# Kernel tuning notes

Measured on AMD Instinct MI355X. Metric: run time of the kernel, lower is better.

## Reference

```python
import jax, jax.numpy as jnp
import numpy as np

E = 1024      # embedding_size
H = 16        # num_head
DQ = DK = DV = 64  # per-head q/k/v size


def setup_inputs() -> dict:
    key = jax.random.key(0)
    ks = jax.random.split(key, 9)
    B, S = 2, 2048
    s = 1.0 / np.sqrt(E)
    return {
        "q": jax.random.normal(ks[0], (B, S, E), jnp.float32),
        "k": jax.random.normal(ks[1], (B, S, E), jnp.float32),
        "v": jax.random.normal(ks[2], (B, S, E), jnp.float32),
        "w_q": jax.random.normal(ks[3], (E, H * DQ), jnp.float32) * s,
        "b_q": jax.random.normal(ks[4], (H * DQ,), jnp.float32) * s,
        "w_k": jax.random.normal(ks[5], (E, H * DK), jnp.float32) * s,
        "b_k": jax.random.normal(ks[6], (H * DK,), jnp.float32) * s,
        "w_v": jax.random.normal(ks[7], (E, H * DV), jnp.float32) * s,
        "b_v": jax.random.normal(ks[8], (H * DV,), jnp.float32) * s,
    }


def reference(q, k, v, w_q, b_q, w_k, b_k, w_v, b_v):
    B, Sq, _ = q.shape
    Sk = k.shape[1]
    # projections -> [B, S, H, d] -> [B, H, S, d]
    qh = (q @ w_q + b_q).reshape(B, Sq, H, DQ).transpose(0, 2, 1, 3)
    kh = (k @ w_k + b_k).reshape(B, Sk, H, DK).transpose(0, 2, 1, 3)
    vh = (v @ w_v + b_v).reshape(B, Sk, H, DV).transpose(0, 2, 1, 3)
    # scaled dot-product attention; scores [B, H, Sq, Sk]
    scores = jnp.einsum("bhqd,bhkd->bhqk", qh, kh) / jnp.sqrt(jnp.float32(DQ))
    weights = jax.nn.softmax(scores, axis=-1)
    out = jnp.einsum("bhqk,bhkd->bhqd", weights, vh)  # [B, H, Sq, DV]
    return out.transpose(0, 2, 1, 3).reshape(B, Sq, H * DV)
```

## Files before the change

### kernel.cpp

```cpp
#include <hip/hip_runtime.h>
#include <hip/hip_bf16.h>

typedef __bf16 bf16_t;
typedef bf16_t bf16x8 __attribute__((ext_vector_type(8)));
typedef bf16_t bf16x4 __attribute__((ext_vector_type(4)));
typedef short  short4v __attribute__((ext_vector_type(4)));
typedef float  f32x4  __attribute__((ext_vector_type(4)));

#define MFMA16(a,b,c) __builtin_amdgcn_mfma_f32_16x16x32_bf16(a, b, c, 0, 0, 0)

static __device__ inline f32x4 mfma_k16(bf16x4 a, bf16x4 b, f32x4 c) {
#if __has_builtin(__builtin_amdgcn_mfma_f32_16x16x16_bf16)
  return __builtin_amdgcn_mfma_f32_16x16x16_bf16(a, b, c, 0, 0, 0);
#else
  return __builtin_amdgcn_mfma_f32_16x16x16bf16_1k(
      __builtin_bit_cast(short4v, a), __builtin_bit_cast(short4v, b), c, 0, 0, 0);
#endif
}

constexpr int S = 2048, H = 16, Dh = 64;
constexpr int N = H * Dh;
constexpr int K = 1024;
constexpr float QSCALE = 0.125f * 1.4426950408889634f;

static __device__ inline void load_lds16(const bf16_t* g, bf16_t* l) {
  __builtin_amdgcn_global_load_lds(
      (const __attribute__((address_space(1))) void*)g,
      (__attribute__((address_space(3))) void*)l, 16, 0, 0);
}

static __device__ inline ushort f2bb(float x) {
  bf16_t h = (bf16_t)x;
  return __builtin_bit_cast(ushort, h);
}

__global__ __launch_bounds__(256) void prep(
    const float* __restrict__ q, const float* __restrict__ k,
    const float* __restrict__ v,
    const float* __restrict__ wq, const float* __restrict__ wk,
    const float* __restrict__ wv,
    bf16_t* __restrict__ xq, bf16_t* __restrict__ xk, bf16_t* __restrict__ xv,
    bf16_t* __restrict__ wtq, bf16_t* __restrict__ wtk, bf16_t* __restrict__ wtv) {
  __shared__ ushort tile[64][68];
  int bx = blockIdx.x, t = threadIdx.x;
  if (bx < 6144) {
    int z = bx >> 11, bb = bx & 2047;
    const float* xi = z == 0 ? q : z == 1 ? k : v;
    bf16_t*      xo = z == 0 ? xq : z == 1 ? xk : xv;
    size_t idx = ((size_t)bb * 256 + t) * 8;
    float4 a = *(const float4*)&xi[idx];
    float4 b = *(const float4*)&xi[idx + 4];
    bf16x8 w;
    w[0] = (bf16_t)a.x; w[1] = (bf16_t)a.y; w[2] = (bf16_t)a.z; w[3] = (bf16_t)a.w;
    w[4] = (bf16_t)b.x; w[5] = (bf16_t)b.y; w[6] = (bf16_t)b.z; w[7] = (bf16_t)b.w;
    *(bf16x8*)&xo[idx] = w;
  } else {
    int zz = bx - 6144;
    int z = zz >> 8, bb = zz & 255;
    const float* wi = z == 0 ? wq : z == 1 ? wk : wv;
    ushort*      wo = (ushort*)(z == 0 ? wtq : z == 1 ? wtk : wtv);
    int k0 = (bb >> 4) * 64, n0 = (bb & 15) * 64;
    for (int i = 0; i < 4; ++i) {
      int idx4 = (i * 256 + t) * 4;
      int r = idx4 >> 6, c = idx4 & 63;
      float4 vv = *(const float4*)&wi[(size_t)(k0 + r) * N + n0 + c];
      tile[r][c] = f2bb(vv.x); tile[r][c + 1] = f2bb(vv.y);
      tile[r][c + 2] = f2bb(vv.z); tile[r][c + 3] = f2bb(vv.w);
    }
    __syncthreads();
    for (int i = 0; i < 4; ++i) {
      int idx4 = (i * 256 + t) * 4;
      int r = idx4 >> 6, c = idx4 & 63;
      ushort4 vv;
      vv.x = tile[c][r]; vv.y = tile[c + 1][r];
      vv.z = tile[c + 2][r]; vv.w = tile[c + 3][r];
      *(ushort4*)&wo[(size_t)(n0 + r) * K + k0 + c] = vv;
    }
  }
}

__global__ __launch_bounds__(256) void proj_gemm(
    const bf16_t* __restrict__ xq, const bf16_t* __restrict__ xk,
    const bf16_t* __restrict__ xv,
    const bf16_t* __restrict__ wtq, const bf16_t* __restrict__ wtk,
    const bf16_t* __restrict__ wtv,
    const float* __restrict__ bq, const float* __restrict__ bk,
    const float* __restrict__ bv,
    bf16_t* __restrict__ qh, bf16_t* __restrict__ kh, bf16_t* __restrict__ vt) {
  int mode = blockIdx.z;
  const bf16_t* X  = mode == 0 ? xq  : mode == 1 ? xk  : wtv;
  const bf16_t* Wt = mode == 0 ? wtq : mode == 1 ? wtk : xv;
  const float*  Bi = mode == 0 ? bq  : mode == 1 ? bk  : bv;

  __shared__ __align__(16) bf16_t smem[17408];
  bf16_t (*Ash)[64] = (bf16_t(*)[64])smem;
  bf16_t (*Bsh)[64] = (bf16_t(*)[64])(smem + 8192);
  bf16_t* Cs = smem;

  int tid = threadIdx.x;
  int wave = tid >> 6, lane = tid & 63;
  int lr = lane & 15, lg = lane >> 4;
  int lrow = lane >> 3, lchunk = lane & 7;
  int m0 = (mode < 2 ? blockIdx.y : blockIdx.x) * 128;
  int n0 = (mode < 2 ? blockIdx.x : blockIdx.y) * 128;
  int wm = (wave >> 1) * 64, wn = (wave & 1) * 64;

  f32x4 acc[4][4];
  for (int i = 0; i < 4; ++i)
    for (int j = 0; j < 4; ++j) acc[i][j] = (f32x4){0.f, 0.f, 0.f, 0.f};

  for (int ko = 0; ko < K / 64; ++ko) {
    __syncthreads();
    for (int j = 0; j < 4; ++j) {
      int r = wave * 32 + j * 8 + lrow;
      int gc = (lchunk ^ (r & 7)) * 8;
      load_lds16(&X [(size_t)(m0 + r) * K + ko * 64 + gc], &Ash[r][lchunk * 8]);
      load_lds16(&Wt[(size_t)(n0 + r) * K + ko * 64 + gc], &Bsh[r][lchunk * 8]);
    }
    __syncthreads();
    for (int kk = 0; kk < 2; ++kk) {
      bf16x8 af[4], bfr[4];
      for (int i = 0; i < 4; ++i) {
        int rr = wm + i * 16 + lr;
        af[i] = *(const bf16x8*)&Ash[rr][(((kk << 2) | lg) ^ (rr & 7)) * 8];
      }
      for (int j = 0; j < 4; ++j) {
        int rr = wn + j * 16 + lr;
        bfr[j] = *(const bf16x8*)&Bsh[rr][(((kk << 2) | lg) ^ (rr & 7)) * 8];
      }
      for (int i = 0; i < 4; ++i)
        for (int j = 0; j < 4; ++j)
          acc[i][j] = MFMA16(af[i], bfr[j], acc[i][j]);
    }
  }

  float badd[4][4][4];
  if (mode < 2) {
    float bvv[4];
    for (int j = 0; j < 4; ++j) bvv[j] = Bi[n0 + wn + j * 16 + lr];
    for (int i = 0; i < 4; ++i)
      for (int j = 0; j < 4; ++j)
        for (int r = 0; r < 4; ++r) badd[i][j][r] = bvv[j];
  } else {
    for (int i = 0; i < 4; ++i)
      for (int r = 0; r < 4; ++r) {
        float bm = Bi[m0 + wm + i * 16 + lg * 4 + r];
        for (int j = 0; j < 4; ++j) badd[i][j][r] = bm;
      }
  }

  __syncthreads();
  for (int i = 0; i < 4; ++i)
    for (int j = 0; j < 4; ++j)
      for (int r = 0; r < 4; ++r) {
        float vvv = acc[i][j][r] + badd[i][j][r];
        if (mode == 0) vvv *= QSCALE;
        Cs[(size_t)(wm + i * 16 + lg * 4 + r) * 136 + wn + j * 16 + lr] = (bf16_t)vvv;
      }
  __syncthreads();

  bf16_t* o = mode == 0 ? qh : mode == 1 ? kh : vt;
  for (int p = 0; p < 8; ++p) {
    int idx = p * 256 + tid;
    int row = idx >> 4, ch = idx & 15;
    bf16x8 vv = *(const bf16x8*)&Cs[(size_t)row * 136 + ch * 8];
    size_t dst;
    if (mode < 2) {
      int m_g = m0 + row, n_g = n0 + ch * 8;
      int b = m_g >> 11, s = m_g & 2047;
      int h = n_g >> 6, d = n_g & 63;
      dst = (((size_t)(b * 16 + h) * 2048) + s) * 64 + d;
    } else {
      int w_g = m0 + row, t_g = n0 + ch * 8;
      int b = t_g >> 11, s = t_g & 2047;
      dst = ((size_t)(b * 1024 + w_g)) * 2048 + s;
    }
    *(uint4*)&o[dst] = __builtin_bit_cast(uint4, vv);
  }
}

__global__ __launch_bounds__(256) void attn(
    const bf16_t* __restrict__ qh, const bf16_t* __restrict__ kh,
    const bf16_t* __restrict__ vt, float* __restrict__ out) {
  __shared__ __align__(16) bf16_t smem[8192];
  bf16_t* kt = smem;
  bf16_t* vs = smem + 4096;

  int tid = threadIdx.x, wave = tid >> 6, lane = tid & 63;
  int lr = lane & 15, lg = lane >> 4;
  int lrow = lane >> 3, lchunk = lane & 7;
  int bh = blockIdx.y;
  int q0 = blockIdx.x * 128 + wave * 32;

  const bf16_t* qg = qh + (size_t)bh * S * Dh;
  const bf16_t* kg = kh + (size_t)bh * S * Dh;
  const bf16_t* vg = vt + (size_t)bh * Dh * S;

  bf16x8 bqf[2][2];
  for (int ms = 0; ms < 2; ++ms)
    for (int kk = 0; kk < 2; ++kk)
      bqf[ms][kk] = *(const bf16x8*)&qg[(size_t)(q0 + ms * 16 + lr) * 64 + kk * 32 + lg * 8];

  bf16x4 ones;
  ones[0] = (bf16_t)1.0f; ones[1] = (bf16_t)1.0f;
  ones[2] = (bf16_t)1.0f; ones[3] = (bf16_t)1.0f;

  f32x4 o_acc[2][4], lacc[2];
  for (int ms = 0; ms < 2; ++ms) {
    lacc[ms] = (f32x4){0.f, 0.f, 0.f, 0.f};
    for (int t = 0; t < 4; ++t) o_acc[ms][t] = (f32x4){0.f, 0.f, 0.f, 0.f};
  }

  int srow0 = wave * 16 + lrow;
  int srow1 = srow0 + 8;
  int sgc = (lchunk ^ (srow0 & 7)) * 8;
  int ld0 = srow0 * 64 + lchunk * 8;
  int ld1 = srow1 * 64 + lchunk * 8;

  uint4 kr0 = *(const uint4*)&kg[(size_t)srow0 * 64 + sgc];
  uint4 kr1 = *(const uint4*)&kg[(size_t)srow1 * 64 + sgc];
  uint4 vr0 = *(const uint4*)&vg[(size_t)srow0 * S + sgc];
  uint4 vr1 = *(const uint4*)&vg[(size_t)srow1 * S + sgc];

  constexpr int NIT = S / 64;
  for (int it = 0; it < NIT; ++it) {
    __syncthreads();
    *(uint4*)&kt[ld0] = kr0;
    *(uint4*)&kt[ld1] = kr1;
    *(uint4*)&vs[ld0] = vr0;
    *(uint4*)&vs[ld1] = vr1;
    if (it + 1 < NIT) {
      int sk1 = (it + 1) * 64;
      kr0 = *(const uint4*)&kg[(size_t)(sk1 + srow0) * 64 + sgc];
      kr1 = *(const uint4*)&kg[(size_t)(sk1 + srow1) * 64 + sgc];
      vr0 = *(const uint4*)&vg[(size_t)srow0 * S + sk1 + sgc];
      vr1 = *(const uint4*)&vg[(size_t)srow1 * S + sk1 + sgc];
    }
    __syncthreads();

    bf16x8 ak[4][2];
    for (int t = 0; t < 4; ++t)
      for (int kk = 0; kk < 2; ++kk)
        ak[t][kk] = *(const bf16x8*)
            &kt[(t * 16 + lr) * 64 + ((kk * 4 + lg) ^ (lr & 7)) * 8];
    bf16x4 bv[4][4];
    for (int t = 0; t < 4; ++t)
      for (int dt = 0; dt < 4; ++dt)
        bv[t][dt] = *(const bf16x4*)
            &vs[(dt * 16 + lr) * 64 + (((t * 2 + (lg >> 1)) ^ (lr & 7)) * 8) + (lg & 1) * 4];

    for (int ms = 0; ms < 2; ++ms) {
      f32x4 st[4];
      for (int t = 0; t < 4; ++t) st[t] = (f32x4){0.f, 0.f, 0.f, 0.f};
      for (int t = 0; t < 4; ++t)
        for (int kk = 0; kk < 2; ++kk)
          st[t] = MFMA16(ak[t][kk], bqf[ms][kk], st[t]);

      bf16x4 pa[4];
      for (int t = 0; t < 4; ++t)
        for (int r = 0; r < 4; ++r)
          pa[t][r] = (bf16_t)__builtin_amdgcn_exp2f(st[t][r]);

      for (int t = 0; t < 4; ++t) {
        for (int dt = 0; dt < 4; ++dt)
          o_acc[ms][dt] = mfma_k16(pa[t], bv[t][dt], o_acc[ms][dt]);
        lacc[ms] = mfma_k16(pa[t], ones, lacc[ms]);
      }
    }
  }

  int b = bh >> 4, h = bh & 15;
  for (int ms = 0; ms < 2; ++ms)
    for (int r = 0; r < 4; ++r) {
      float inv = 1.f / lacc[ms][r];
      int s_row = q0 + ms * 16 + lg * 4 + r;
      size_t base = ((size_t)(b * S + s_row)) * 1024 + h * 64;
      for (int dt = 0; dt < 4; ++dt)
        out[base + dt * 16 + lr] = o_acc[ms][dt][r] * inv;
    }
}

extern "C" void kernel_launch(void* const* d_in, const int* in_sizes, int n_in,
                              void* d_out, int out_size, void* d_ws, size_t ws_size,
                              hipStream_t stream) {
  const float* q  = (const float*)d_in[0];
  const float* k  = (const float*)d_in[1];
  const float* v  = (const float*)d_in[2];
  const float* wq = (const float*)d_in[3];
  const float* bq = (const float*)d_in[4];
  const float* wk = (const float*)d_in[5];
  const float* bk = (const float*)d_in[6];
  const float* wv = (const float*)d_in[7];
  const float* bv = (const float*)d_in[8];

  bf16_t* ws  = (bf16_t*)d_ws;
  constexpr size_t MW = (size_t)1 << 20;
  constexpr size_t MX = (size_t)4096 * 1024;
  bf16_t* wtq = ws;
  bf16_t* wtk = wtq + MW;
  bf16_t* wtv = wtk + MW;
  bf16_t* xq  = wtv + MW;
  bf16_t* xk  = xq + MX;
  bf16_t* xv  = xk + MX;
  bf16_t* qhd = xv + MX;
  bf16_t* khd = qhd + MX;
  bf16_t* vtd = khd + MX;
  float* out  = (float*)d_out;

  prep<<<6912, 256, 0, stream>>>(q, k, v, wq, wk, wv,
                                 xq, xk, xv, wtq, wtk, wtv);
  proj_gemm<<<dim3(8, 32, 3), 256, 0, stream>>>(xq, xk, xv, wtq, wtk, wtv,
                                                bq, bk, bv, qhd, khd, vtd);
  attn<<<dim3(16, 32), 256, 0, stream>>>(qhd, khd, vtd, out);
}
```

Baseline: 207.9 us.

## Use 8 waves with 16 query rows each and K=32 MFMAs for PV

The attention kernel now runs 512 threads (8 waves), each owning 16 query rows instead of 32. Each thread stages one K and one V chunk per tile instead of two. The P·V and row-sum products switch from 16x16x16 MFMAs to 16x16x32 MFMAs by packing two key sub-tiles into one bf16x8 operand, which halves the MFMA instruction count for that stage. In exchange, K and V fragments are reread from LDS with less reuse per wave, and each block carries more waves.

```diff
diff --git a/kernel.cpp b/kernel.cpp
--- a/kernel.cpp
+++ b/kernel.cpp
@@ -8,15 +8,6 @@
 typedef float  f32x4  __attribute__((ext_vector_type(4)));
 
 #define MFMA16(a,b,c) __builtin_amdgcn_mfma_f32_16x16x32_bf16(a, b, c, 0, 0, 0)
-
-static __device__ inline f32x4 mfma_k16(bf16x4 a, bf16x4 b, f32x4 c) {
-#if __has_builtin(__builtin_amdgcn_mfma_f32_16x16x16_bf16)
-  return __builtin_amdgcn_mfma_f32_16x16x16_bf16(a, b, c, 0, 0, 0);
-#else
-  return __builtin_amdgcn_mfma_f32_16x16x16bf16_1k(
-      __builtin_bit_cast(short4v, a), __builtin_bit_cast(short4v, b), c, 0, 0, 0);
-#endif
-}
 
 constexpr int S = 2048, H = 16, Dh = 64;
 constexpr int N = H * Dh;
@@ -179,7 +170,7 @@
   }
 }
 
-__global__ __launch_bounds__(256) void attn(
+__global__ __launch_bounds__(512) void attn(
     const bf16_t* __restrict__ qh, const bf16_t* __restrict__ kh,
     const bf16_t* __restrict__ vt, float* __restrict__ out) {
   __shared__ __align__(16) bf16_t smem[8192];
@@ -188,53 +179,42 @@
 
   int tid = threadIdx.x, wave = tid >> 6, lane = tid & 63;
   int lr = lane & 15, lg = lane >> 4;
-  int lrow = lane >> 3, lchunk = lane & 7;
   int bh = blockIdx.y;
-  int q0 = blockIdx.x * 128 + wave * 32;
+  int q0 = blockIdx.x * 128 + wave * 16;
 
   const bf16_t* qg = qh + (size_t)bh * S * Dh;
   const bf16_t* kg = kh + (size_t)bh * S * Dh;
   const bf16_t* vg = vt + (size_t)bh * Dh * S;
 
-  bf16x8 bqf[2][2];
-  for (int ms = 0; ms < 2; ++ms)
-    for (int kk = 0; kk < 2; ++kk)
-      bqf[ms][kk] = *(const bf16x8*)&qg[(size_t)(q0 + ms * 16 + lr) * 64 + kk * 32 + lg * 8];
-
-  bf16x4 ones;
-  ones[0] = (bf16_t)1.0f; ones[1] = (bf16_t)1.0f;
-  ones[2] = (bf16_t)1.0f; ones[3] = (bf16_t)1.0f;
-
-  f32x4 o_acc[2][4], lacc[2];
-  for (int ms = 0; ms < 2; ++ms) {
-    lacc[ms] = (f32x4){0.f, 0.f, 0.f, 0.f};
-    for (int t = 0; t < 4; ++t) o_acc[ms][t] = (f32x4){0.f, 0.f, 0.f, 0.f};
-  }
-
-  int srow0 = wave * 16 + lrow;
-  int srow1 = srow0 + 8;
-  int sgc = (lchunk ^ (srow0 & 7)) * 8;
-  int ld0 = srow0 * 64 + lchunk * 8;
-  int ld1 = srow1 * 64 + lchunk * 8;
-
-  uint4 kr0 = *(const uint4*)&kg[(size_t)srow0 * 64 + sgc];
-  uint4 kr1 = *(const uint4*)&kg[(size_t)srow1 * 64 + sgc];
-  uint4 vr0 = *(const uint4*)&vg[(size_t)srow0 * S + sgc];
-  uint4 vr1 = *(const uint4*)&vg[(size_t)srow1 * S + sgc];
+  bf16x8 bqf[2];
+  for (int kk = 0; kk < 2; ++kk)
+    bqf[kk] = *(const bf16x8*)&qg[(size_t)(q0 + lr) * 64 + kk * 32 + lg * 8];
+
+  bf16x8 ones8;
+  for (int j = 0; j < 8; ++j) ones8[j] = (bf16_t)1.0f;
+
+  f32x4 o_acc[4], lacc;
+  lacc = (f32x4){0.f, 0.f, 0.f, 0.f};
+  for (int dt = 0; dt < 4; ++dt) o_acc[dt] = (f32x4){0.f, 0.f, 0.f, 0.f};
+
+  int srow = tid >> 3, schunk = tid & 7;
+  int sgc = (schunk ^ (srow & 7)) * 8;
+  int ld = srow * 64 + schunk * 8;
+
+  uint4 kr = *(const uint4*)&kg[(size_t)srow * 64 + sgc];
+  uint4 vr = *(const uint4*)&vg[(size_t)srow * S + sgc];
+
+  int sw = lr & 7, p4 = (lg & 1) * 4;
 
   constexpr int NIT = S / 64;
   for (int it = 0; it < NIT; ++it) {
     __syncthreads();
-    *(uint4*)&kt[ld0] = kr0;
-    *(uint4*)&kt[ld1] = kr1;
-    *(uint4*)&vs[ld0] = vr0;
-    *(uint4*)&vs[ld1] = vr1;
+    *(uint4*)&kt[ld] = kr;
+    *(uint4*)&vs[ld] = vr;
     if (it + 1 < NIT) {
       int sk1 = (it + 1) * 64;
-      kr0 = *(const uint4*)&kg[(size_t)(sk1 + srow0) * 64 + sgc];
-      kr1 = *(const uint4*)&kg[(size_t)(sk1 + srow1) * 64 + sgc];
-      vr0 = *(const uint4*)&vg[(size_t)srow0 * S + sk1 + sgc];
-      vr1 = *(const uint4*)&vg[(size_t)srow1 * S + sk1 + sgc];
+      kr = *(const uint4*)&kg[(size_t)(sk1 + srow) * 64 + sgc];
+      vr = *(const uint4*)&vg[(size_t)srow * S + sk1 + sgc];
     }
     __syncthreads();
 
@@ -242,42 +222,44 @@
     for (int t = 0; t < 4; ++t)
       for (int kk = 0; kk < 2; ++kk)
         ak[t][kk] = *(const bf16x8*)
-            &kt[(t * 16 + lr) * 64 + ((kk * 4 + lg) ^ (lr & 7)) * 8];
-    bf16x4 bv[4][4];
-    for (int t = 0; t < 4; ++t)
+            &kt[(t * 16 + lr) * 64 + ((kk * 4 + lg) ^ sw) * 8];
+
+    f32x4 st[4];
+    for (int t = 0; t < 4; ++t) st[t] = (f32x4){0.f, 0.f, 0.f, 0.f};
+    for (int kk = 0; kk < 2; ++kk)
+      for (int t = 0; t < 4; ++t)
+        st[t] = MFMA16(ak[t][kk], bqf[kk], st[t]);
+
+    bf16x8 pa8[2];
+    for (int tp = 0; tp < 2; ++tp)
+      for (int r = 0; r < 4; ++r) {
+        pa8[tp][r]     = (bf16_t)__builtin_amdgcn_exp2f(st[2 * tp][r]);
+        pa8[tp][r + 4] = (bf16_t)__builtin_amdgcn_exp2f(st[2 * tp + 1][r]);
+      }
+
+    for (int tp = 0; tp < 2; ++tp) {
+      int g0 = tp * 4 + (lg >> 1);
+      bf16x8 bb[4];
+      for (int dt = 0; dt < 4; ++dt) {
+        const bf16_t* vrow = &vs[(dt * 16 + lr) * 64];
+        bf16x4 lo = *(const bf16x4*)&vrow[((g0      ^ sw) * 8) + p4];
+        bf16x4 hi = *(const bf16x4*)&vrow[(((g0 + 2) ^ sw) * 8) + p4];
+        for (int j = 0; j < 4; ++j) { bb[dt][j] = lo[j]; bb[dt][j + 4] = hi[j]; }
+      }
       for (int dt = 0; dt < 4; ++dt)
-        bv[t][dt] = *(const bf16x4*)
-            &vs[(dt * 16 + lr) * 64 + (((t * 2 + (lg >> 1)) ^ (lr & 7)) * 8) + (lg & 1) * 4];
-
-    for (int ms = 0; ms < 2; ++ms) {
-      f32x4 st[4];
-      for (int t = 0; t < 4; ++t) st[t] = (f32x4){0.f, 0.f, 0.f, 0.f};
-      for (int t = 0; t < 4; ++t)
-        for (int kk = 0; kk < 2; ++kk)
-          st[t] = MFMA16(ak[t][kk], bqf[ms][kk], st[t]);
-
-      bf16x4 pa[4];
-      for (int t = 0; t < 4; ++t)
-        for (int r = 0; r < 4; ++r)
-          pa[t][r] = (bf16_t)__builtin_amdgcn_exp2f(st[t][r]);
-
-      for (int t = 0; t < 4; ++t) {
-        for (int dt = 0; dt < 4; ++dt)
-          o_acc[ms][dt] = mfma_k16(pa[t], bv[t][dt], o_acc[ms][dt]);
-        lacc[ms] = mfma_k16(pa[t], ones, lacc[ms]);
-      }
+        o_acc[dt] = MFMA16(pa8[tp], bb[dt], o_acc[dt]);
+      lacc = MFMA16(pa8[tp], ones8, lacc);
     }
   }
 
   int b = bh >> 4, h = bh & 15;
-  for (int ms = 0; ms < 2; ++ms)
-    for (int r = 0; r < 4; ++r) {
-      float inv = 1.f / lacc[ms][r];
-      int s_row = q0 + ms * 16 + lg * 4 + r;
-      size_t base = ((size_t)(b * S + s_row)) * 1024 + h * 64;
-      for (int dt = 0; dt < 4; ++dt)
-        out[base + dt * 16 + lr] = o_acc[ms][dt][r] * inv;
-    }
+  for (int r = 0; r < 4; ++r) {
+    float inv = 1.f / lacc[r];
+    int s_row = q0 + lg * 4 + r;
+    size_t base = ((size_t)(b * S + s_row)) * 1024 + h * 64;
+    for (int dt = 0; dt < 4; ++dt)
+      out[base + dt * 16 + lr] = o_acc[dt][r] * inv;
+  }
 }
 
 extern "C" void kernel_launch(void* const* d_in, const int* in_sizes, int n_in,
@@ -311,5 +293,5 @@
                                  xq, xk, xv, wtq, wtk, wtv);
   proj_gemm<<<dim3(8, 32, 3), 256, 0, stream>>>(xq, xk, xv, wtq, wtk, wtv,
                                                 bq, bk, bv, qhd, khd, vtd);
-  attn<<<dim3(16, 32), 256, 0, stream>>>(qhd, khd, vtd, out);
-}
+  attn<<<dim3(16, 32), 512, 0, stream>>>(qhd, khd, vtd, out);
+}
```

Result: faster. 203.4 us (-2.2%).
